# Kernel tuning notes

Hardware: AMD Instinct MI355X
Metric: run time of the kernel (lower is better)

The kernel has to match this reference:

```python
import jax, jax.numpy as jnp
import numpy as np

B, S, D, HW = 256, 32, 512, 196


def setup_inputs() -> dict:
    key = jax.random.key(0)
    ks = jax.random.split(key, 34)
    n = lambda k, sh, s=1.0: jax.random.normal(k, sh, dtype=jnp.float32) * s
    w = 0.03  # xavier-ish scale for D=512 layers
    return {
        "words": n(ks[0], (B, S, D)),
        "question": n(ks[1], (B, 2 * D)),
        "know": n(ks[2], (B, D, HW)),
        "control0": n(ks[3], (B, D)),
        "memory0": n(ks[4], (B, D)),
        # ControlUnit
        "Wsc": n(ks[5], (2 * D, D), w), "bsc": jnp.zeros((D,), jnp.float32),
        "Wp": n(ks[6], (D, D), w), "bp": jnp.zeros((D,), jnp.float32),
        "Wcq": n(ks[7], (2 * D, D), w), "bcq": jnp.zeros((D,), jnp.float32),
        "wac": n(ks[8], (D, 1), w), "bac": jnp.zeros((1,), jnp.float32),
        # ReadUnit
        "Wm": n(ks[9], (D, D), w), "bm": jnp.zeros((D,), jnp.float32),
        "Wk": n(ks[10], (D, D), w), "bk": jnp.zeros((D,), jnp.float32),
        "Wc1": n(ks[11], (3 * D, D), w), "bc1": jnp.zeros((D,), jnp.float32),
        "Wc2": n(ks[12], (D, D), w), "bc2": jnp.zeros((D,), jnp.float32),
        "war": n(ks[13], (D, 1), w), "bar": jnp.zeros((1,), jnp.float32),
        # WriteUnit (self-attention variant)
        "Wwc": n(ks[14], (D, D), w), "bwc": jnp.zeros((D,), jnp.float32),
        "waw": n(ks[15], (D, 1), w), "baw": jnp.zeros((1,), jnp.float32),
        "Wwcat": n(ks[16], (3 * D, D), w), "bwcat": jnp.zeros((D,), jnp.float32),
    }


def reference(words, question, know, control0, memory0,
              Wsc, bsc, Wp, bp, Wcq, bcq, wac, bac,
              Wm, bm, Wk, bk, Wc1, bc1, Wc2, bc2, war, bar,
              Wwc, bwc, waw, baw, Wwcat, bwcat):
    # ---- ControlUnit (step 0) ----
    q = jnp.tanh(question @ Wsc + bsc)                    # [B,D]
    pa = q @ Wp + bp                                      # position_aware[0]
    cq = jnp.concatenate([control0, pa], axis=1) @ Wcq + bcq  # [B,D]
    logit_c = (cq[:, None, :] * words) @ wac + bac        # [B,S,1]
    attn_c = jax.nn.softmax(logit_c, axis=1)
    control = jnp.sum(attn_c * words, axis=1)             # [B,D]

    # ---- ReadUnit ----
    pm = memory0 @ Wm + bm                                # [B,D]
    pk = jnp.einsum('bdn,de->ben', know, Wk) + bk[None, :, None]  # [B,D,HW]
    pm_b = jnp.broadcast_to(pm[:, :, None], pk.shape)
    feat = jnp.concatenate([pm_b * pk, pk, pm_b], axis=1)  # [B,3D,HW]
    h = jax.nn.relu(jnp.einsum('bfn,fd->bnd', feat, Wc1) + bc1)  # [B,HW,D]
    h = h @ Wc2 + bc2                                     # [B,HW,D]
    logit_r = (h * control[:, None, :]) @ war + bar       # [B,HW,1]
    a_r = jax.nn.softmax(logit_r[..., 0], axis=1)          # [B,HW]
    read = jnp.einsum('bdn,bn->bd', know, a_r)            # [B,D]

    # ---- WriteUnit (self-attention over previous controls; T=1 at step 0) ----
    sc = control @ Wwc + bwc                              # [B,D]
    ctrl_prev = control0[:, :, None]                      # [B,D,T]
    logit_w = jnp.einsum('bdt,d->bt', sc[:, :, None] * ctrl_prev, waw[:, 0]) + baw  # [B,T]
    a_w = jax.nn.softmax(logit_w, axis=1)
    attn_mem = jnp.einsum('bdt,bt->bd', memory0[:, :, None], a_w)  # [B,D]
    concat = jnp.concatenate([read, memory0, attn_mem], axis=1)    # [B,3D]
    next_mem = concat @ Wwcat + bwcat                     # [B,D]

    return control, next_mem
```

## Files before the change

kernel.cpp:

```cpp
#include <hip/hip_runtime.h>
#include <hip/hip_bf16.h>
#include <math.h>

typedef __hip_bfloat16 bf16;
typedef __attribute__((ext_vector_type(8))) short s8v;
typedef __attribute__((ext_vector_type(4))) float f4v;

#define BB 256
#define SS 32
#define DD 512
#define HWN 196
#define AP 40

__device__ __forceinline__ float b2f(bf16 x){ return __bfloat162float(x); }
__device__ __forceinline__ bf16 f2b(float x){ return __float2bfloat16(x); }
__device__ __forceinline__ float us2f(unsigned short u){
    union { unsigned int i; float f; } t; t.i = ((unsigned int)u) << 16; return t.f;
}
__device__ __forceinline__ float ldin(int dt, const void* p, size_t i){
    return dt ? b2f(((const bf16*)p)[i]) : ((const float*)p)[i];
}

__global__ void detect_k(const void* q, int* flag){
    __shared__ int cnt;
    if (threadIdx.x == 0) cnt = 0;
    __syncthreads();
    const unsigned short* u = (const unsigned short*)q;
    unsigned short v = u[threadIdx.x * 4];
    int e = (v >> 7) & 0xFF;
    atomicAdd(&cnt, (e >= 100 && e <= 140) ? 1 : 0);
    __syncthreads();
    if (threadIdx.x == 0) *flag = (cnt > 128) ? 1 : 0;
}

struct PJob { const void* s; const void* s_b; const void* s2; const void* s2_b;
              bf16* d; int R, C, ldd, kofs, mode, boff; };
struct PrepP { PJob j[11]; const void* war; const void* bk; float* warf; float* bkf; };

__global__ __launch_bounds__(256) void prep_k(PrepP P, const int* __restrict__ flag){
    const int dt = *flag;
    __shared__ float T[32][33];
    int bx = blockIdx.x;
    int ji = 0;
    #pragma unroll
    for (int i = 0; i < 11; ++i) if (bx >= P.j[i].boff) ji = i;
    PJob jb = P.j[ji];
    const void* src  = dt ? jb.s_b  : jb.s;
    const void* src2 = dt ? jb.s2_b : jb.s2;
    int t = bx - jb.boff;
    int tx = threadIdx.x & 31, ty = threadIdx.x >> 5;
    if (jb.mode == 3){
        for (int i = threadIdx.x; i < DD; i += 256){
            P.warf[i] = ldin(dt, P.war, i);
            P.bkf[i]  = ldin(dt, P.bk, i);
        }
        return;
    }
    int nrt = jb.R >> 5;
    int r0 = (t % nrt) << 5, c0 = (t / nrt) << 5;
    if (jb.mode == 2){
        for (int rr = ty; rr < 32; rr += 8)
            jb.d[(size_t)(r0 + rr) * jb.ldd + jb.kofs + c0 + tx] =
                f2b(ldin(dt, src, (size_t)(r0 + rr) * jb.C + c0 + tx));
        return;
    }
    for (int rr = ty; rr < 32; rr += 8){
        float v = ldin(dt, src, (size_t)(r0 + rr) * jb.C + c0 + tx);
        if (jb.mode == 1) v += ldin(dt, src2, (size_t)(r0 + rr) * jb.C + c0 + tx);
        T[rr][tx] = v;
    }
    __syncthreads();
    for (int rr = ty; rr < 32; rr += 8)
        jb.d[(size_t)(c0 + rr) * jb.ldd + jb.kofs + r0 + tx] = f2b(T[tx][rr]);
}

__global__ void tr_know(const void* __restrict__ know, bf16* __restrict__ knowT, int b0,
                        const int* __restrict__ flag){
    const int dt = *flag;
    int bl = blockIdx.z, b = b0 + bl;
    int n0 = blockIdx.x * 32, g0 = blockIdx.y * 32;
    __shared__ float T[32][33];
    int tx = threadIdx.x & 31, ty = threadIdx.x >> 5;
    size_t base = (size_t)b * DD * HWN;
    for (int rr = ty; rr < 32; rr += 8){
        int n = n0 + tx;
        T[rr][tx] = (n < HWN) ? ldin(dt, know, base + (size_t)(g0 + rr) * HWN + n) : 0.f;
    }
    __syncthreads();
    for (int rr = ty; rr < 32; rr += 8){
        int n = n0 + rr;
        if (n < HWN) knowT[((size_t)bl * HWN + n) * DD + g0 + tx] = f2b(T[tx][rr]);
    }
}

__device__ __forceinline__ void tile_decode(int idb, int swz, int& rt, int& ct){
    if (swz){ int g = idb >> 6, w = idb & 63; rt = g * 8 + (w & 7); ct = w >> 3; }
    else    { ct = idb & 7; rt = idb >> 3; }
}

__global__ __launch_bounds__(256) void g1_mfma(const bf16* __restrict__ A,
                                               const bf16* __restrict__ BT,
                                               const float* __restrict__ bkf,
                                               bf16* __restrict__ C, int swz){
    __shared__ __align__(16) bf16 As[128 * AP];
    __shared__ __align__(16) bf16 Bs[64 * AP];
    const int tid = threadIdx.x, lane = tid & 63, wave = tid >> 6;
    const int q = lane >> 4, mr = lane & 15;
    int rt, ct; tile_decode(blockIdx.x, swz, rt, ct);
    const int r0 = rt * 128, c0 = ct * 64;
    f4v acc[2][4];
    #pragma unroll
    for (int t = 0; t < 2; ++t)
        #pragma unroll
        for (int j = 0; j < 4; ++j){ f4v z = {0.f,0.f,0.f,0.f}; acc[t][j] = z; }
    for (int k0 = 0; k0 < DD; k0 += 32){
        #pragma unroll
        for (int cc = 0; cc < 2; ++cc){
            int c = tid + cc * 256;
            int row = c >> 2, ko = (c & 3) * 8;
            *(float4*)&As[row * AP + ko] =
                *(const float4*)(A + (size_t)(r0 + row) * DD + k0 + ko);
        }
        {
            int col = tid >> 2, ko = (tid & 3) * 8;
            *(float4*)&Bs[col * AP + ko] =
                *(const float4*)(BT + (size_t)(c0 + col) * DD + k0 + ko);
        }
        __syncthreads();
        s8v a0 = *(const s8v*)&As[(wave * 32 + mr) * AP + q * 8];
        s8v a1 = *(const s8v*)&As[(wave * 32 + 16 + mr) * AP + q * 8];
        #pragma unroll
        for (int j = 0; j < 4; ++j){
            s8v b = *(const s8v*)&Bs[(j * 16 + mr) * AP + q * 8];
            acc[0][j] = __builtin_amdgcn_mfma_f32_16x16x32_bf16(a0, b, acc[0][j], 0, 0, 0);
            acc[1][j] = __builtin_amdgcn_mfma_f32_16x16x32_bf16(a1, b, acc[1][j], 0, 0, 0);
        }
        __syncthreads();
    }
    #pragma unroll
    for (int t = 0; t < 2; ++t)
        #pragma unroll
        for (int j = 0; j < 4; ++j)
            #pragma unroll
            for (int i = 0; i < 4; ++i){
                int row = r0 + wave * 32 + t * 16 + q * 4 + i;
                int col = c0 + j * 16 + mr;
                C[(size_t)row * DD + col] = f2b(acc[t][j][i] + bkf[col]);
            }
}

__global__ __launch_bounds__(256) void g2_mfma(const bf16* __restrict__ Apk,
                                               const bf16* __restrict__ BT,
                                               const float* __restrict__ pmf,
                                               const float* __restrict__ t3b,
                                               const float* __restrict__ uf,
                                               float* __restrict__ lpart,
                                               int b0, int swz){
    __shared__ __align__(16) bf16 As[128 * AP];
    __shared__ __align__(16) bf16 Bs[64 * AP];
    const int tid = threadIdx.x, lane = tid & 63, wave = tid >> 6;
    const int q = lane >> 4, mr = lane & 15;
    int rt, ct; tile_decode(blockIdx.x, swz, rt, ct);
    const int r0 = rt * 128, c0 = ct * 64;
    f4v acc[2][4];
    #pragma unroll
    for (int t = 0; t < 2; ++t)
        #pragma unroll
        for (int j = 0; j < 4; ++j){ f4v z = {0.f,0.f,0.f,0.f}; acc[t][j] = z; }
    for (int k0 = 0; k0 < 2 * DD; k0 += 32){
        #pragma unroll
        for (int cc = 0; cc < 2; ++cc){
            int c = tid + cc * 256;
            int row = c >> 2, ko = (c & 3) * 8;
            int ksrc = (k0 + ko) & (DD - 1);
            float4 v = *(const float4*)(Apk + (size_t)(r0 + row) * DD + ksrc);
            alignas(16) bf16 h[8];
            *(float4*)h = v;
            if (k0 < DD){
                int b = b0 + (r0 + row) / HWN;
                const float* pp = pmf + (size_t)b * DD + ksrc;
                #pragma unroll
                for (int i2 = 0; i2 < 8; ++i2) h[i2] = f2b(b2f(h[i2]) * pp[i2]);
            }
            *(float4*)&As[row * AP + ko] = *(const float4*)h;
        }
        {
            int col = tid >> 2, ko = (tid & 3) * 8;
            *(float4*)&Bs[col * AP + ko] =
                *(const float4*)(BT + (size_t)(c0 + col) * (2 * DD) + k0 + ko);
        }
        __syncthreads();
        s8v a0 = *(const s8v*)&As[(wave * 32 + mr) * AP + q * 8];
        s8v a1 = *(const s8v*)&As[(wave * 32 + 16 + mr) * AP + q * 8];
        #pragma unroll
        for (int j = 0; j < 4; ++j){
            s8v b = *(const s8v*)&Bs[(j * 16 + mr) * AP + q * 8];
            acc[0][j] = __builtin_amdgcn_mfma_f32_16x16x32_bf16(a0, b, acc[0][j], 0, 0, 0);
            acc[1][j] = __builtin_amdgcn_mfma_f32_16x16x32_bf16(a1, b, acc[1][j], 0, 0, 0);
        }
        __syncthreads();
    }
    float part[2][4] = {};
    #pragma unroll
    for (int t = 0; t < 2; ++t)
        #pragma unroll
        for (int j = 0; j < 4; ++j)
            #pragma unroll
            for (int i = 0; i < 4; ++i){
                int row = r0 + wave * 32 + t * 16 + q * 4 + i;
                int b = b0 + row / HWN;
                int col = c0 + j * 16 + mr;
                float hv = acc[t][j][i] + t3b[(size_t)b * DD + col];
                part[t][i] += fmaxf(hv, 0.f) * uf[(size_t)b * DD + col];
            }
    #pragma unroll
    for (int t = 0; t < 2; ++t)
        #pragma unroll
        for (int i = 0; i < 4; ++i){
            float v = part[t][i];
            v += __shfl_xor(v, 1, 16);
            v += __shfl_xor(v, 2, 16);
            v += __shfl_xor(v, 4, 16);
            v += __shfl_xor(v, 8, 16);
            if (mr == 0){
                int row = r0 + wave * 32 + t * 16 + q * 4 + i;
                lpart[(size_t)ct * (BB * HWN) + (size_t)b0 * HWN + row] = v;
            }
        }
}

__global__ void reduce_logit_k(const float* __restrict__ lpart, const float* __restrict__ bias_r,
                               float* __restrict__ logit){
    int i = blockIdx.x * 256 + threadIdx.x;
    const int T = BB * HWN;
    if (i < T){
        float s = bias_r[i / HWN];
        #pragma unroll
        for (int c = 0; c < 8; ++c) s += lpart[(size_t)c * T + i];
        logit[i] = s;
    }
}

struct SSeg { const void* A; int a_ws, lda, K, koff; };
struct SP {
    SSeg s[2]; int nseg;
    const bf16* BT; int ldb;
    const float* amul;
    const void* bias;
    float* C; int M, N, act;
};

__global__ __launch_bounds__(256) void sgemm_k(SP p, const int* __restrict__ flag){
    const int dt = *flag;
    const int tid = threadIdx.x, lane = tid & 63, w = tid >> 6;
    const int q = lane >> 4, mr = lane & 15;
    const int n0 = blockIdx.x * 16, m0 = blockIdx.y * 64 + w * 16;
    f4v acc = {0.f,0.f,0.f,0.f};
    for (int sg = 0; sg < p.nseg; ++sg){
        const SSeg s = p.s[sg];
        const float* amul = (sg == 0) ? p.amul : nullptr;
        #pragma unroll 4
        for (int k0 = 0; k0 < s.K; k0 += 32){
            const int kk = k0 + q * 8;
            union { bf16 h[8]; s8v v; } a;
            if (s.a_ws || dt == 0){
                const float* Af = (const float*)s.A + (size_t)(m0 + mr) * s.lda + kk;
                float4 f0 = *(const float4*)Af;
                float4 f1 = *(const float4*)(Af + 4);
                float f[8] = {f0.x, f0.y, f0.z, f0.w, f1.x, f1.y, f1.z, f1.w};
                if (amul){
                    #pragma unroll
                    for (int j = 0; j < 8; ++j) f[j] *= amul[kk + j];
                }
                #pragma unroll
                for (int j = 0; j < 8; ++j) a.h[j] = f2b(f[j]);
            } else {
                a.v = *(const s8v*)((const bf16*)s.A + (size_t)(m0 + mr) * s.lda + kk);
                if (amul){
                    #pragma unroll
                    for (int j = 0; j < 8; ++j) a.h[j] = f2b(b2f(a.h[j]) * amul[kk + j]);
                }
            }
            s8v b = *(const s8v*)(p.BT + (size_t)(n0 + mr) * p.ldb + s.koff + kk);
            acc = __builtin_amdgcn_mfma_f32_16x16x32_bf16(a.v, b, acc, 0, 0, 0);
        }
    }
    #pragma unroll
    for (int i = 0; i < 4; ++i){
        int row = m0 + q * 4 + i, col = n0 + mr;
        float v = acc[i] + (p.bias ? ldin(dt, p.bias, col) : 0.f);
        if (p.act == 1) v = tanhf(v);
        p.C[(size_t)row * p.N + col] = v;
    }
}

__global__ __launch_bounds__(256) void attn_control_k(const float* __restrict__ cq,
                                                      const void* __restrict__ wac,
                                                      const void* __restrict__ bac,
                                                      const void* __restrict__ words,
                                                      float* __restrict__ control,
                                                      const int* __restrict__ flag){
    const int dt = *flag;
    const int b = blockIdx.x, tid = threadIdx.x;
    __shared__ float cw[DD];
    __shared__ float lg[SS];
    __shared__ float es[SS];
    for (int d = tid; d < DD; d += 256) cw[d] = cq[(size_t)b*DD + d] * ldin(dt, wac, d);
    __syncthreads();
    int s = tid >> 3, l8 = tid & 7;
    float p = 0.f;
    for (int d = l8; d < DD; d += 8) p += cw[d] * ldin(dt, words, ((size_t)b*SS + s)*DD + d);
    for (int off = 4; off; off >>= 1) p += __shfl_down(p, off, 8);
    if (l8 == 0) lg[s] = p + ldin(dt, bac, 0);
    __syncthreads();
    if (tid == 0){
        float mx = -INFINITY;
        for (int i = 0; i < SS; ++i) mx = fmaxf(mx, lg[i]);
        float sm = 0.f;
        for (int i = 0; i < SS; ++i){ es[i] = expf(lg[i] - mx); sm += es[i]; }
        float inv = 1.f / sm;
        for (int i = 0; i < SS; ++i) es[i] *= inv;
    }
    __syncthreads();
    for (int d = tid; d < DD; d += 256){
        float c = 0.f;
        #pragma unroll 8
        for (int s2 = 0; s2 < SS; ++s2) c += es[s2] * ldin(dt, words, ((size_t)b*SS + s2)*DD + d);
        control[(size_t)b*DD + d] = c;
    }
}

__global__ __launch_bounds__(256) void vbias_k(const float* __restrict__ control,
                                               const void* __restrict__ war,
                                               const void* __restrict__ bc2,
                                               const void* __restrict__ bar,
                                               float* __restrict__ bias_r,
                                               const int* __restrict__ flag){
    const int dt = *flag;
    const int b = blockIdx.x, tid = threadIdx.x;
    __shared__ float red[256];
    float p = 0.f;
    for (int d = tid; d < DD; d += 256)
        p += ldin(dt, bc2, d) * control[(size_t)b*DD + d] * ldin(dt, war, d);
    red[tid] = p; __syncthreads();
    for (int off = 128; off; off >>= 1){ if (tid < off) red[tid] += red[tid + off]; __syncthreads(); }
    if (tid == 0) bias_r[b] = red[0] + ldin(dt, bar, 0);
}

__global__ __launch_bounds__(256) void softmax_read_k(const float* __restrict__ logit,
                                                      const void* __restrict__ know,
                                                      float* __restrict__ readout,
                                                      const int* __restrict__ flag){
    const int dt = *flag;
    const int b = blockIdx.x, tid = threadIdx.x;
    __shared__ float a[HWN];
    __shared__ float red[256];
    float x = (tid < HWN) ? logit[(size_t)b*HWN + tid] : -INFINITY;
    red[tid] = x; __syncthreads();
    for (int off = 128; off; off >>= 1){ if (tid < off) red[tid] = fmaxf(red[tid], red[tid + off]); __syncthreads(); }
    float mx = red[0]; __syncthreads();
    float e = (tid < HWN) ? expf(x - mx) : 0.f;
    red[tid] = e; __syncthreads();
    for (int off = 128; off; off >>= 1){ if (tid < off) red[tid] += red[tid + off]; __syncthreads(); }
    float inv = 1.f / red[0];
    if (tid < HWN) a[tid] = e * inv;
    __syncthreads();
    for (int d = tid; d < DD; d += 256){
        size_t base = ((size_t)b*DD + d) * HWN;
        float sum = 0.f;
        if (dt){
            const ushort4* k4 = (const ushort4*)((const unsigned short*)know + base);
            #pragma unroll 7
            for (int c = 0; c < HWN/4; ++c){
                ushort4 u4 = k4[c];
                sum += a[4*c+0]*us2f(u4.x) + a[4*c+1]*us2f(u4.y)
                     + a[4*c+2]*us2f(u4.z) + a[4*c+3]*us2f(u4.w);
            }
        } else {
            const float4* k4 = (const float4*)((const float*)know + base);
            #pragma unroll 7
            for (int c = 0; c < HWN/4; ++c){
                float4 f4 = k4[c];
                sum += a[4*c+0]*f4.x + a[4*c+1]*f4.y + a[4*c+2]*f4.z + a[4*c+3]*f4.w;
            }
        }
        readout[(size_t)b*DD + d] = sum;
    }
}

__global__ void writeout_k(const float* __restrict__ control, const float* __restrict__ nm,
                           void* __restrict__ out, const int* __restrict__ flag){
    const int dt = *flag;
    int i = blockIdx.x * 256 + threadIdx.x;
    const int NBD = BB * DD;
    float v;
    if (i < NBD) v = control[i];
    else if (i < 2*NBD) v = nm[i - NBD];
    else return;
    if (dt) ((bf16*)out)[i] = f2b(v);
    else    ((float*)out)[i] = v;
}

extern "C" void kernel_launch(void* const* d_in, const int* in_sizes, int n_in,
                              void* d_out, int out_size, void* d_ws, size_t ws_size,
                              hipStream_t stream){
    const void* words    = d_in[0];
    const void* question = d_in[1];
    const void* know     = d_in[2];
    const void* control0 = d_in[3];
    const void* memory0  = d_in[4];
    const void* Wsc = d_in[5];   const void* bsc = d_in[6];
    const void* Wp  = d_in[7];   const void* bp  = d_in[8];
    const void* Wcq = d_in[9];   const void* bcq = d_in[10];
    const void* wac = d_in[11];  const void* bac = d_in[12];
    const void* Wm  = d_in[13];  const void* bm  = d_in[14];
    const void* Wk  = d_in[15];  const void* bk  = d_in[16];
    const void* Wc1 = d_in[17];  const void* bc1 = d_in[18];
    const void* Wc2 = d_in[19];  const void* bc2 = d_in[20];
    const void* war = d_in[21];  const void* bar = d_in[22];
    const void* Wwcat = d_in[27]; const void* bwcat = d_in[28];

    int* flag = (int*)d_ws;
    float* F = ((float*)d_ws) + 16;
    const int NBD = BB * DD;
    float* q_   = F;
    float* pa   = F + 1*NBD;
    float* cq   = F + 2*NBD;
    float* ctrl = F + 3*NBD;
    float* pm   = F + 4*NBD;
    float* t3b  = F + 5*NBD;
    float* u_   = F + 6*NBD;
    float* rd   = F + 7*NBD;
    float* nm   = F + 8*NBD;
    float* bias_r = F + 9*NBD;
    float* logit  = bias_r + BB;
    float* warf   = logit + BB*HWN;
    float* bkf    = warf + DD;
    float* lpart  = bkf + DD;
    size_t off_f = 16 + 9*(size_t)NBD + BB + (size_t)BB*HWN + 2*DD + 8*(size_t)BB*HWN;
    size_t byte_off = (off_f * 4 + 255) & ~(size_t)255;
    bf16* WB = (bf16*)((char*)d_ws + byte_off);
    bf16* WscT   = WB;
    bf16* WcqT   = WscT  + (size_t)DD*2*DD;
    bf16* Wc1T2  = WcqT  + (size_t)DD*2*DD;
    bf16* WwcatF = Wc1T2 + (size_t)DD*2*DD;
    bf16* WpT    = WwcatF+ (size_t)DD*2*DD;
    bf16* WmT    = WpT   + (size_t)DD*DD;
    bf16* Wc1t3T = WmT   + (size_t)DD*DD;
    bf16* WkT    = Wc1t3T+ (size_t)DD*DD;
    bf16* Wc2cv  = WkT   + (size_t)DD*DD;
    size_t big_off = (byte_off + ((size_t)DD*2*DD*4 + (size_t)DD*DD*5) * sizeof(bf16) + 255) & ~(size_t)255;

    size_t per_batch = (size_t)HWN * DD * sizeof(bf16) * 2;
    size_t avail = (ws_size > big_off) ? (ws_size - big_off) : 0;
    int CB = (int)(avail / per_batch);
    CB &= ~31;
    if (CB > BB) CB = BB;
    if (CB < 32) CB = 32;
    bf16* knowT = (bf16*)((char*)d_ws + big_off);
    bf16* pkT   = knowT + (size_t)CB * HWN * DD;

    dim3 blk(256);

    detect_k<<<dim3(1), blk, 0, stream>>>(question, flag);

    {
        PrepP P; int bo = 0;
        auto J = [&](const void* s, const void* sb, const void* s2, const void* s2b,
                     bf16* d, int R, int C, int ldd, int kofs, int mode, int idx){
            int nb = (mode == 3) ? 1 : ((R >> 5) * (C >> 5));
            P.j[idx] = PJob{ s, sb, s2, s2b, d, R, C, ldd, kofs, mode, bo };
            bo += nb;
        };
        const void* Wc1t3_f = (const void*)((const float*)Wc1 + (size_t)2*DD*DD);
        const void* Wc1t3_b = (const void*)((const bf16*) Wc1 + (size_t)2*DD*DD);
        const void* Ww1_f = (const void*)((const float*)Wwcat + (size_t)DD*DD);
        const void* Ww1_b = (const void*)((const bf16*) Wwcat + (size_t)DD*DD);
        const void* Ww2_f = (const void*)((const float*)Wwcat + (size_t)2*DD*DD);
        const void* Ww2_b = (const void*)((const bf16*) Wwcat + (size_t)2*DD*DD);
        J(Wsc,   Wsc,   nullptr, nullptr, WscT,   2*DD, DD, 2*DD, 0,   0, 0);
        J(Wp,    Wp,    nullptr, nullptr, WpT,    DD,   DD, DD,   0,   0, 1);
        J(Wcq,   Wcq,   nullptr, nullptr, WcqT,   2*DD, DD, 2*DD, 0,   0, 2);
        J(Wm,    Wm,    nullptr, nullptr, WmT,    DD,   DD, DD,   0,   0, 3);
        J(Wc1,   Wc1,   nullptr, nullptr, Wc1T2,  2*DD, DD, 2*DD, 0,   0, 4);
        J(Wc1t3_f, Wc1t3_b, nullptr, nullptr, Wc1t3T, DD, DD, DD, 0,   0, 5);
        J(Wk,    Wk,    nullptr, nullptr, WkT,    DD,   DD, DD,   0,   0, 6);
        J(Wwcat, Wwcat, nullptr, nullptr, WwcatF, DD,   DD, 2*DD, 0,   0, 7);
        J(Ww1_f, Ww1_b, Ww2_f,   Ww2_b,   WwcatF, DD,   DD, 2*DD, 512, 1, 8);
        J(Wc2,   Wc2,   nullptr, nullptr, Wc2cv,  DD,   DD, DD,   0,   2, 9);
        J(nullptr,nullptr,nullptr,nullptr,nullptr,0,    0,  0,    0,   3, 10);
        P.war = war; P.bk = bk; P.warf = warf; P.bkf = bkf;
        prep_k<<<dim3(bo), blk, 0, stream>>>(P, flag);
    }

    dim3 g_s(DD/16, BB/64);
    SP p;

    p = SP{}; p.nseg = 1;
    p.s[0] = SSeg{ question, 0, 2*DD, 2*DD, 0 };
    p.BT = WscT; p.ldb = 2*DD; p.amul = nullptr;
    p.bias = bsc; p.C = q_; p.M = BB; p.N = DD; p.act = 1;
    sgemm_k<<<g_s, blk, 0, stream>>>(p, flag);
    p = SP{}; p.nseg = 1;
    p.s[0] = SSeg{ q_, 1, DD, DD, 0 };
    p.BT = WpT; p.ldb = DD; p.amul = nullptr;
    p.bias = bp; p.C = pa; p.M = BB; p.N = DD; p.act = 0;
    sgemm_k<<<g_s, blk, 0, stream>>>(p, flag);
    p = SP{}; p.nseg = 2;
    p.s[0] = SSeg{ control0, 0, DD, DD, 0 };
    p.s[1] = SSeg{ pa,       1, DD, DD, 512 };
    p.BT = WcqT; p.ldb = 2*DD; p.amul = nullptr;
    p.bias = bcq; p.C = cq; p.M = BB; p.N = DD; p.act = 0;
    sgemm_k<<<g_s, blk, 0, stream>>>(p, flag);
    attn_control_k<<<dim3(BB), blk, 0, stream>>>(cq, wac, bac, words, ctrl, flag);
    p = SP{}; p.nseg = 1;
    p.s[0] = SSeg{ memory0, 0, DD, DD, 0 };
    p.BT = WmT; p.ldb = DD; p.amul = nullptr;
    p.bias = bm; p.C = pm; p.M = BB; p.N = DD; p.act = 0;
    sgemm_k<<<g_s, blk, 0, stream>>>(p, flag);
    p = SP{}; p.nseg = 1;
    p.s[0] = SSeg{ pm, 1, DD, DD, 0 };
    p.BT = Wc1t3T; p.ldb = DD; p.amul = nullptr;
    p.bias = bc1; p.C = t3b; p.M = BB; p.N = DD; p.act = 0;
    sgemm_k<<<g_s, blk, 0, stream>>>(p, flag);
    vbias_k<<<dim3(BB), blk, 0, stream>>>(ctrl, war, bc2, bar, bias_r, flag);
    p = SP{}; p.nseg = 1;
    p.s[0] = SSeg{ ctrl, 1, DD, DD, 0 };
    p.BT = Wc2cv; p.ldb = DD; p.amul = warf;
    p.bias = nullptr; p.C = u_; p.M = BB; p.N = DD; p.act = 0;
    sgemm_k<<<g_s, blk, 0, stream>>>(p, flag);

    for (int b0 = 0; b0 < BB; b0 += CB){
        int cb = (b0 + CB <= BB) ? CB : (BB - b0);
        int M = cb * HWN;
        dim3 g_tr((HWN + 31)/32, DD/32, cb);
        tr_know<<<g_tr, blk, 0, stream>>>(know, knowT, b0, flag);
        int nR = M / 128;
        int swz = (nR % 8 == 0) ? 1 : 0;
        dim3 gflat(8 * nR);
        g1_mfma<<<gflat, blk, 0, stream>>>(knowT, WkT, bkf, pkT, swz);
        g2_mfma<<<gflat, blk, 0, stream>>>(pkT, Wc1T2, pm, t3b, u_, lpart, b0, swz);
    }

    reduce_logit_k<<<dim3((BB*HWN + 255)/256), blk, 0, stream>>>(lpart, bias_r, logit);
    softmax_read_k<<<dim3(BB), blk, 0, stream>>>(logit, know, rd, flag);
    p = SP{}; p.nseg = 2;
    p.s[0] = SSeg{ rd,      1, DD, DD, 0 };
    p.s[1] = SSeg{ memory0, 0, DD, DD, 512 };
    p.BT = WwcatF; p.ldb = 2*DD; p.amul = nullptr;
    p.bias = bwcat; p.C = nm; p.M = BB; p.N = DD; p.act = 0;
    sgemm_k<<<g_s, blk, 0, stream>>>(p, flag);
    writeout_k<<<dim3(2*NBD/256), blk, 0, stream>>>(ctrl, nm, d_out, flag);
}
```

Before: 633.6 us.

## Fold per-batch memory scaling into weights to halve g2 GEMM K dimension

The second GEMM previously ran over K=2D, concatenating pm*pk and pk against two weight halves. It now uses (pm ⊙ W1 + W2) as a per-batch effective weight, so K drops to D, and it tiles by batch, with each batch's 196 rows padded into two 128-row tiles. This removes half the MFMA work and the per-element A scaling, but builds the weight tile per block from two weight loads plus a pm load, and pads rows from 196 to 256 per batch.

New measurement: 575.1 us. 1.1x faster.

```diff
diff --git a/kernel.cpp b/kernel.cpp
--- a/kernel.cpp
+++ b/kernel.cpp
@@ -160,43 +160,52 @@
     __shared__ __align__(16) bf16 Bs[64 * AP];
     const int tid = threadIdx.x, lane = tid & 63, wave = tid >> 6;
     const int q = lane >> 4, mr = lane & 15;
-    int rt, ct; tile_decode(blockIdx.x, swz, rt, ct);
-    const int r0 = rt * 128, c0 = ct * 64;
+    int idb = blockIdx.x, u, ct;
+    if (swz){ int g = idb >> 6, w = idb & 63; u = g * 8 + (w & 7); ct = w >> 3; }
+    else    { u = idb >> 3; ct = idb & 7; }
+    const int bl = u >> 1, rt = u & 1;
+    const int b = b0 + bl;
+    const int c0 = ct * 64, rbase = rt * 128;
+    const float* pmb = pmf + (size_t)b * DD;
     f4v acc[2][4];
     #pragma unroll
     for (int t = 0; t < 2; ++t)
         #pragma unroll
         for (int j = 0; j < 4; ++j){ f4v z = {0.f,0.f,0.f,0.f}; acc[t][j] = z; }
-    for (int k0 = 0; k0 < 2 * DD; k0 += 32){
+    for (int k0 = 0; k0 < DD; k0 += 32){
         #pragma unroll
         for (int cc = 0; cc < 2; ++cc){
             int c = tid + cc * 256;
             int row = c >> 2, ko = (c & 3) * 8;
-            int ksrc = (k0 + ko) & (DD - 1);
-            float4 v = *(const float4*)(Apk + (size_t)(r0 + row) * DD + ksrc);
-            alignas(16) bf16 h[8];
-            *(float4*)h = v;
-            if (k0 < DD){
-                int b = b0 + (r0 + row) / HWN;
-                const float* pp = pmf + (size_t)b * DD + ksrc;
-                #pragma unroll
-                for (int i2 = 0; i2 < 8; ++i2) h[i2] = f2b(b2f(h[i2]) * pp[i2]);
-            }
-            *(float4*)&As[row * AP + ko] = *(const float4*)h;
+            int rl = rbase + row;
+            float4 v = {0.f, 0.f, 0.f, 0.f};
+            if (rl < HWN)
+                v = *(const float4*)(Apk + ((size_t)bl * HWN + rl) * DD + k0 + ko);
+            *(float4*)&As[row * AP + ko] = v;
         }
         {
             int col = tid >> 2, ko = (tid & 3) * 8;
-            *(float4*)&Bs[col * AP + ko] =
-                *(const float4*)(BT + (size_t)(c0 + col) * (2 * DD) + k0 + ko);
+            const bf16* wrow = BT + (size_t)(c0 + col) * (2 * DD) + k0 + ko;
+            union { bf16 h[8]; float4 f; } w1, w2, be;
+            w1.f = *(const float4*)wrow;
+            w2.f = *(const float4*)(wrow + DD);
+            float4 pA = *(const float4*)(pmb + k0 + ko);
+            float4 pB = *(const float4*)(pmb + k0 + ko + 4);
+            #pragma unroll
+            for (int j = 0; j < 4; ++j){
+                be.h[j]     = f2b((&pA.x)[j] * b2f(w1.h[j])     + b2f(w2.h[j]));
+                be.h[4 + j] = f2b((&pB.x)[j] * b2f(w1.h[4 + j]) + b2f(w2.h[4 + j]));
+            }
+            *(float4*)&Bs[col * AP + ko] = be.f;
         }
         __syncthreads();
         s8v a0 = *(const s8v*)&As[(wave * 32 + mr) * AP + q * 8];
         s8v a1 = *(const s8v*)&As[(wave * 32 + 16 + mr) * AP + q * 8];
         #pragma unroll
         for (int j = 0; j < 4; ++j){
-            s8v b = *(const s8v*)&Bs[(j * 16 + mr) * AP + q * 8];
-            acc[0][j] = __builtin_amdgcn_mfma_f32_16x16x32_bf16(a0, b, acc[0][j], 0, 0, 0);
-            acc[1][j] = __builtin_amdgcn_mfma_f32_16x16x32_bf16(a1, b, acc[1][j], 0, 0, 0);
+            s8v b2 = *(const s8v*)&Bs[(j * 16 + mr) * AP + q * 8];
+            acc[0][j] = __builtin_amdgcn_mfma_f32_16x16x32_bf16(a0, b2, acc[0][j], 0, 0, 0);
+            acc[1][j] = __builtin_amdgcn_mfma_f32_16x16x32_bf16(a1, b2, acc[1][j], 0, 0, 0);
         }
         __syncthreads();
     }
@@ -207,11 +216,12 @@
         for (int j = 0; j < 4; ++j)
             #pragma unroll
             for (int i = 0; i < 4; ++i){
-                int row = r0 + wave * 32 + t * 16 + q * 4 + i;
-                int b = b0 + row / HWN;
-                int col = c0 + j * 16 + mr;
-                float hv = acc[t][j][i] + t3b[(size_t)b * DD + col];
-                part[t][i] += fmaxf(hv, 0.f) * uf[(size_t)b * DD + col];
+                int rl = rbase + wave * 32 + t * 16 + q * 4 + i;
+                if (rl < HWN){
+                    int col = c0 + j * 16 + mr;
+                    float hv = acc[t][j][i] + t3b[(size_t)b * DD + col];
+                    part[t][i] += fmaxf(hv, 0.f) * uf[(size_t)b * DD + col];
+                }
             }
     #pragma unroll
     for (int t = 0; t < 2; ++t)
@@ -222,10 +232,9 @@
             v += __shfl_xor(v, 2, 16);
             v += __shfl_xor(v, 4, 16);
             v += __shfl_xor(v, 8, 16);
-            if (mr == 0){
-                int row = r0 + wave * 32 + t * 16 + q * 4 + i;
-                lpart[(size_t)ct * (BB * HWN) + (size_t)b0 * HWN + row] = v;
-            }
+            int rl = rbase + wave * 32 + t * 16 + q * 4 + i;
+            if (mr == 0 && rl < HWN)
+                lpart[(size_t)ct * (BB * HWN) + (size_t)b * HWN + rl] = v;
         }
 }
 
@@ -536,10 +545,11 @@
         dim3 g_tr((HWN + 31)/32, DD/32, cb);
         tr_know<<<g_tr, blk, 0, stream>>>(know, knowT, b0, flag);
         int nR = M / 128;
-        int swz = (nR % 8 == 0) ? 1 : 0;
-        dim3 gflat(8 * nR);
-        g1_mfma<<<gflat, blk, 0, stream>>>(knowT, WkT, bkf, pkT, swz);
-        g2_mfma<<<gflat, blk, 0, stream>>>(pkT, Wc1T2, pm, t3b, u_, lpart, b0, swz);
+        int swz1 = (nR % 8 == 0) ? 1 : 0;
+        g1_mfma<<<dim3(8 * nR), blk, 0, stream>>>(knowT, WkT, bkf, pkT, swz1);
+        int nU = cb * 2;
+        int swz2 = (nU % 8 == 0) ? 1 : 0;
+        g2_mfma<<<dim3(8 * nU), blk, 0, stream>>>(pkT, Wc1T2, pm, t3b, u_, lpart, b0, swz2);
     }
 
     reduce_logit_k<<<dim3((BB*HWN + 255)/256), blk, 0, stream>>>(lpart, bias_r, logit);
```
